# Kernel optimization log

Measured on AMD Instinct MI355X. Metric: run time of the kernel, lower is better.

The kernel has to match this reference:

```python
import jax, jax.numpy as jnp
import numpy as np

BS, NUM_VISIT, MAX_FEAT, MAX_TARGET = 32, 6, 12, 16
NUM_FEAT, NUM_REL, HIDDEN, REDUCED, OUT = 1992, 11, 128, 256, 90
GAMMA = 0.1


def setup_inputs() -> dict:
    key = jax.random.key(0)
    ks = jax.random.split(key, 20)
    u = lambda k, shape: jax.random.uniform(k, shape, dtype=jnp.float32)
    # one/multi-hot-like dense float inputs (per docstring)
    feat_index = (u(ks[0], (BS, NUM_VISIT, MAX_FEAT, NUM_FEAT)) < 0.01).astype(jnp.float32)
    neighbor_index = (u(ks[1], (BS, NUM_VISIT, MAX_FEAT, MAX_TARGET, NUM_FEAT)) < 0.001).astype(jnp.float32)
    rel_index = (u(ks[2], (BS, NUM_VISIT, MAX_FEAT, MAX_TARGET, NUM_REL)) < 0.2).astype(jnp.float32)
    # parameters (torch.rand init in the original; xavier for embedding)
    bound = float(np.sqrt(6.0 / (NUM_FEAT + HIDDEN)))
    emb_weight = jax.random.uniform(ks[3], (NUM_FEAT, HIDDEN), dtype=jnp.float32, minval=-bound, maxval=bound)
    return {
        "feat_index": feat_index,
        "neighbor_index": neighbor_index,
        "rel_index": rel_index,
        "emb_weight": emb_weight,
        "W_edge": u(ks[4], (NUM_REL, HIDDEN)),
        "W_v": u(ks[5], (REDUCED, HIDDEN)),
        "W_r": u(ks[6], (REDUCED, HIDDEN)),
        "b_v": u(ks[7], (REDUCED,)),
        "b_r": u(ks[8], (REDUCED,)),
        "W_alpha": u(ks[9], (NUM_FEAT,)),
        "b_alpha": u(ks[10], (MAX_FEAT,)),
        "W_beta": u(ks[11], (MAX_FEAT,)),
        "b_beta": u(ks[12], (NUM_VISIT,)),
        "W_l": u(ks[13], (REDUCED, REDUCED)),
        "b_l": u(ks[14], (REDUCED,)),
        "fc_W": u(ks[15], (OUT, 2 * REDUCED)) * 0.05,
        "fc_b": u(ks[16], (OUT,)) * 0.05,
    }


def reference(feat_index, neighbor_index, rel_index, emb_weight, W_edge, W_v, W_r,
              b_v, b_r, W_alpha, b_alpha, W_beta, b_beta, W_l, b_l, fc_W, fc_b):
    num_visit = feat_index.shape[1]
    # decay buffer lamb[i] = exp(-gamma*(num_visit - i))
    lamb = jnp.exp(-GAMMA * (num_visit - jnp.arange(num_visit, dtype=feat_index.dtype)))

    # node-level attention alpha: (b,v,m)
    alpha = jax.nn.softmax(jnp.einsum('n,bvmn->bvm', W_alpha, feat_index) + b_alpha)
    # visit-level attention beta: (b,v), modulated by temporal decay
    beta = jnp.tanh(jnp.einsum('m,bvm->bv', W_beta, alpha) + b_beta) * lamb

    # reduced node embeddings: (num_feat, reduced)
    reduced_emb = emb_weight @ W_v.T + b_v
    # attention-weighted neighbor aggregation; sum over targets t fused in
    attn = alpha * beta[:, :, None]                       # (b,v,m)
    node_agg = jnp.einsum('bvm,bvmtn,nr->bvmr', attn, neighbor_index, reduced_emb)

    # reduced edge (relation) embeddings: (num_rel, reduced)
    reduced_edge = W_edge @ W_r.T + b_r
    edge_agg = jnp.einsum('bvmtr,rd->bvmd', rel_index, reduced_edge)  # sum over t fused

    agg = node_agg + edge_agg                             # (b,v,m,reduced)
    # einsum('dd, bvfd -> bvfd') in torch takes the diagonal of W_l
    h = jax.nn.relu(jnp.diagonal(W_l) * agg + b_l)        # (b,v,m,reduced)

    h_g = h.sum(axis=(1, 2))                              # (b, reduced)
    # einsum('bvmn,bvmr->bvnr').sum(n).sum(v) == contract over v,m,n
    h_p = jnp.einsum('bvm,bvmr->br', feat_index.sum(-1), h)

    z_joint = jnp.concatenate([h_g, h_p], axis=-1)        # (b, 2*reduced)
    return jax.nn.sigmoid(z_joint @ fc_W.T + fc_b)
```

## Files before the change

kernel.cpp:

```cpp
#include <hip/hip_runtime.h>
#include <math.h>

#define BS   32
#define NV   6
#define MF   12
#define MT   16
#define NF   1992
#define NR   11
#define HID  128
#define RED  256
#define OUTD 90
#define GAMMA 0.1f
#define NZCAP 1024

typedef float f4_t __attribute__((ext_vector_type(4)));

#define WS_HG    0
#define WS_HP    (WS_HG + BS*RED)
#define WS_ATTN  (WS_HP + BS*RED)
#define WS_FSUM  (WS_ATTN + BS*NV*MF)
#define WS_REMB  (WS_FSUM + BS*NV*MF)
#define WS_REDGE (WS_REMB + NF*RED)
#define WS_WTV   (WS_REDGE + NR*RED)
#define WS_WTR   (WS_WTV + HID*RED)
#define WS_FCWT  (WS_WTR + HID*RED)
#define WS_DIAG  (WS_FCWT + 2*RED*OUTD)
#define WS_CNT   (WS_DIAG + RED)
#define WS_RSUM  (WS_CNT + BS*NV*MF)
#define WS_NZN   (WS_RSUM + BS*NV*MF*NR)
#define WS_NZV   (WS_NZN + BS*NV*MF*NZCAP)

#define STREAM_BLOCKS (BS*NV*MF)
#define N_ZERO (2*BS*RED)
#define N_WTV  (HID*RED)
#define N_WTR  (HID*RED)
#define N_FCWT (2*RED*OUTD)
#define N_DIAG RED
#define PREP_ELEMS (N_ZERO + N_WTV + N_WTR + N_FCWT + N_DIAG)
#define PREP_BLOCKS (PREP_ELEMS / 256)

__global__ __launch_bounds__(256) void k_stream_prep_attn(
        const float* __restrict__ nbr, const float* __restrict__ rel,
        const float* __restrict__ W_v, const float* __restrict__ W_r,
        const float* __restrict__ fc_W, const float* __restrict__ W_l,
        const float* __restrict__ feat, const float* __restrict__ W_alpha,
        const float* __restrict__ b_alpha, const float* __restrict__ W_beta,
        const float* __restrict__ b_beta,
        float* __restrict__ ws_base,
        float* __restrict__ WT_v, float* __restrict__ WT_r, float* __restrict__ fcWT,
        float* __restrict__ diag,
        int* __restrict__ cnt_g, float* __restrict__ rsum_g,
        int* __restrict__ nzn_g, float* __restrict__ nzv_g,
        float* __restrict__ attn_ws, float* __restrict__ fsum_ws) {
    int blk = blockIdx.x;
    int tid = threadIdx.x;

    if (blk < STREAM_BLOCKS) {
        int bvm = blk;
        __shared__ int   nz_n[NZCAP];
        __shared__ float nz_v[NZCAP];
        __shared__ float relbuf[MT * NR];
        __shared__ int   cnt;
        if (tid == 0) cnt = 0;
        if (tid < MT * NR / 4) {
            ((f4_t*)relbuf)[tid] = ((const f4_t*)(rel + (size_t)bvm * MT * NR))[tid];
        }

        const f4_t* base = (const f4_t*)(nbr + (size_t)bvm * MT * NF);
        f4_t x[8];
        f4_t a0 = (f4_t)(0.f);
        f4_t a1 = (f4_t)(0.f);
        #pragma unroll
        for (int t = 0; t < 8; ++t) x[t] = __builtin_nontemporal_load(base + t * (NF/4) + tid);
        #pragma unroll
        for (int t = 0; t < 8; ++t) a0 += x[t];
        #pragma unroll
        for (int t = 0; t < 8; ++t) x[t] = __builtin_nontemporal_load(base + (t + 8) * (NF/4) + tid);
        #pragma unroll
        for (int t = 0; t < 8; ++t) a0 += x[t];
        const bool has1 = (tid + 256) < (NF / 4);
        if (has1) {
            #pragma unroll
            for (int t = 0; t < 8; ++t) x[t] = __builtin_nontemporal_load(base + t * (NF/4) + tid + 256);
            #pragma unroll
            for (int t = 0; t < 8; ++t) a1 += x[t];
            #pragma unroll
            for (int t = 0; t < 8; ++t) x[t] = __builtin_nontemporal_load(base + (t + 8) * (NF/4) + tid + 256);
            #pragma unroll
            for (int t = 0; t < 8; ++t) a1 += x[t];
        }
        __syncthreads();

        int nb = tid * 4;
        #pragma unroll
        for (int c = 0; c < 4; ++c)
            if (a0[c] != 0.f) {
                int p = atomicAdd(&cnt, 1);
                if (p < NZCAP) { nz_n[p] = nb + c; nz_v[p] = a0[c]; }
            }
        if (has1) {
            nb = (tid + 256) * 4;
            #pragma unroll
            for (int c = 0; c < 4; ++c)
                if (a1[c] != 0.f) {
                    int p = atomicAdd(&cnt, 1);
                    if (p < NZCAP) { nz_n[p] = nb + c; nz_v[p] = a1[c]; }
                }
        }
        __syncthreads();
        int c = min(cnt, NZCAP);
        if (tid == 0) cnt_g[bvm] = c;
        if (tid < NR) {
            float rs = 0.f;
            #pragma unroll
            for (int t = 0; t < MT; ++t) rs += relbuf[t * NR + tid];
            rsum_g[bvm * NR + tid] = rs;
        }
        for (int i = tid; i < c; i += 256) {
            nzn_g[bvm * NZCAP + i] = nz_n[i];
            nzv_g[bvm * NZCAP + i] = nz_v[i];
        }
        return;
    }
    blk -= STREAM_BLOCKS;

    if (blk < PREP_BLOCKS) {
        int i = blk * 256 + tid;
        if (i < N_ZERO) {
            ws_base[i] = 0.f;
        } else if (i < N_ZERO + N_WTV) {
            int j = i - N_ZERO;
            int k = j >> 8, r = j & 255;
            WT_v[j] = W_v[r * HID + k];
        } else if (i < N_ZERO + N_WTV + N_WTR) {
            int j = i - (N_ZERO + N_WTV);
            int k = j >> 8, r = j & 255;
            WT_r[j] = W_r[r * HID + k];
        } else if (i < N_ZERO + N_WTV + N_WTR + N_FCWT) {
            int j = i - (N_ZERO + N_WTV + N_WTR);
            int jj = j / OUTD, o = j - jj * OUTD;
            fcWT[j] = fc_W[o * (2 * RED) + jj];
        } else {
            int j = i - (N_ZERO + N_WTV + N_WTR + N_FCWT);
            diag[j] = W_l[(size_t)j * RED + j];
        }
        return;
    }

    int bv   = blk - PREP_BLOCKS;
    int v    = bv % NV;
    int wave = tid >> 6;
    int lane = tid & 63;
    __shared__ float dot12[MF], fs12[MF];
    const float* base = feat + (size_t)bv * MF * NF;
    for (int m = wave; m < MF; m += 4) {
        const float4* rw = (const float4*)(base + (size_t)m * NF);
        const float4* wa = (const float4*)W_alpha;
        float da = 0.f, fs = 0.f;
        for (int i = lane; i < NF / 4; i += 64) {
            float4 x = rw[i];
            float4 w = wa[i];
            da += w.x * x.x + w.y * x.y + w.z * x.z + w.w * x.w;
            fs += x.x + x.y + x.z + x.w;
        }
        #pragma unroll
        for (int off = 32; off > 0; off >>= 1) {
            da += __shfl_xor(da, off);
            fs += __shfl_xor(fs, off);
        }
        if (lane == 0) { dot12[m] = da; fs12[m] = fs; }
    }
    __syncthreads();
    if (tid == 0) {
        float logits[MF];
        float mx = -1e30f;
        for (int m = 0; m < MF; ++m) { logits[m] = dot12[m] + b_alpha[m]; mx = fmaxf(mx, logits[m]); }
        float s = 0.f;
        for (int m = 0; m < MF; ++m) { logits[m] = expf(logits[m] - mx); s += logits[m]; }
        float inv = 1.f / s;
        float bdot = 0.f;
        for (int m = 0; m < MF; ++m) { logits[m] *= inv; bdot += W_beta[m] * logits[m]; }
        float lamb = expf(-GAMMA * (float)(NV - v));
        float beta = tanhf(bdot + b_beta[v]) * lamb;
        for (int m = 0; m < MF; ++m) {
            attn_ws[bv * MF + m] = logits[m] * beta;
            fsum_ws[bv * MF + m] = fs12[m];
        }
    }
}

#define NPB 8
#define NODE_BLOCKS (NF / NPB)
__global__ __launch_bounds__(256) void k_reduce(
        const float* __restrict__ emb, const float* __restrict__ W_edge,
        const float* __restrict__ WT_v, const float* __restrict__ WT_r,
        const float* __restrict__ b_v, const float* __restrict__ b_r,
        float* __restrict__ remb, float* __restrict__ redge) {
    int blk = blockIdx.x;
    int tid = threadIdx.x;
    if (blk < NODE_BLOCKS) {
        __shared__ float rows[NPB][HID];
        int n0 = blk * NPB;
        for (int i = tid; i < NPB * HID; i += 256)
            rows[i >> 7][i & 127] = emb[(size_t)n0 * HID + i];
        __syncthreads();
        float bv0 = b_v[tid];
        float a0 = bv0, a1 = bv0, a2 = bv0, a3 = bv0;
        float a4 = bv0, a5 = bv0, a6 = bv0, a7 = bv0;
        #pragma unroll 4
        for (int k = 0; k < HID; ++k) {
            float w = WT_v[k * RED + tid];
            a0 += rows[0][k] * w;
            a1 += rows[1][k] * w;
            a2 += rows[2][k] * w;
            a3 += rows[3][k] * w;
            a4 += rows[4][k] * w;
            a5 += rows[5][k] * w;
            a6 += rows[6][k] * w;
            a7 += rows[7][k] * w;
        }
        float* dst = remb + (size_t)n0 * RED + tid;
        dst[0*RED] = a0; dst[1*RED] = a1; dst[2*RED] = a2; dst[3*RED] = a3;
        dst[4*RED] = a4; dst[5*RED] = a5; dst[6*RED] = a6; dst[7*RED] = a7;
    } else {
        int e = blk - NODE_BLOCKS;
        __shared__ float row[HID];
        if (tid < HID) row[tid] = W_edge[e * HID + tid];
        __syncthreads();
        float acc = b_r[tid];
        #pragma unroll 4
        for (int k = 0; k < HID; ++k)
            acc += row[k] * WT_r[k * RED + tid];
        redge[e * RED + tid] = acc;
    }
}

__global__ __launch_bounds__(256) void k_gather(
        const float* __restrict__ remb, const float* __restrict__ redge,
        const int* __restrict__ cnt_g, const float* __restrict__ rsum_g,
        const int* __restrict__ nzn_g, const float* __restrict__ nzv_g,
        const float* __restrict__ attn_ws, const float* __restrict__ fsum_ws,
        const float* __restrict__ diag, const float* __restrict__ b_l,
        float* __restrict__ h_g, float* __restrict__ h_p) {
    int bvm = blockIdx.x;
    int b   = bvm / (NV * MF);
    int tid = threadIdx.x;
    __shared__ int   nz_n[NZCAP];
    __shared__ float nz_v[NZCAP];
    __shared__ float rsum[NR];
    int c = cnt_g[bvm];
    if (tid < NR) rsum[tid] = rsum_g[bvm * NR + tid];
    for (int i = tid; i < c; i += 256) {
        nz_n[i] = nzn_g[bvm * NZCAP + i];
        nz_v[i] = nzv_g[bvm * NZCAP + i];
    }
    __syncthreads();
    int r = tid;
    float node = 0.f;
    for (int i = 0; i < c; ++i)
        node += nz_v[i] * remb[(size_t)nz_n[i] * RED + r];
    float edge = 0.f;
    #pragma unroll
    for (int j = 0; j < NR; ++j)
        edge += rsum[j] * redge[j * RED + r];
    float a  = attn_ws[bvm];
    float fs = fsum_ws[bvm];
    float agg = a * node + edge;
    float h = fmaxf(0.f, diag[r] * agg + b_l[r]);
    atomicAdd(&h_g[b * RED + r], h);
    atomicAdd(&h_p[b * RED + r], fs * h);
}

__global__ __launch_bounds__(256) void k_out(
        const float* __restrict__ h_g, const float* __restrict__ h_p,
        const float* __restrict__ fcWT, const float* __restrict__ fc_b,
        float* __restrict__ out) {
    int b   = blockIdx.x;
    int tid = threadIdx.x;
    __shared__ float z[2 * RED];
    __shared__ float part[2][OUTD];
    for (int j = tid; j < RED; j += 256) {
        z[j]       = h_g[b * RED + j];
        z[RED + j] = h_p[b * RED + j];
    }
    __syncthreads();
    int o = tid & 127, half = tid >> 7;
    if (o < OUTD) {
        float acc = 0.f;
        int j0 = half * RED;
        #pragma unroll 8
        for (int j = j0; j < j0 + RED; ++j)
            acc += z[j] * fcWT[j * OUTD + o];
        part[half][o] = acc;
    }
    __syncthreads();
    if (tid < OUTD) {
        float acc = part[0][tid] + part[1][tid] + fc_b[tid];
        out[b * OUTD + tid] = 1.f / (1.f + expf(-acc));
    }
}

extern "C" void kernel_launch(void* const* d_in, const int* in_sizes, int n_in,
                              void* d_out, int out_size, void* d_ws, size_t ws_size,
                              hipStream_t stream) {
    const float* feat    = (const float*)d_in[0];
    const float* nbr     = (const float*)d_in[1];
    const float* rel     = (const float*)d_in[2];
    const float* emb     = (const float*)d_in[3];
    const float* W_edge  = (const float*)d_in[4];
    const float* W_v     = (const float*)d_in[5];
    const float* W_r     = (const float*)d_in[6];
    const float* b_v     = (const float*)d_in[7];
    const float* b_r     = (const float*)d_in[8];
    const float* W_alpha = (const float*)d_in[9];
    const float* b_alpha = (const float*)d_in[10];
    const float* W_beta  = (const float*)d_in[11];
    const float* b_beta  = (const float*)d_in[12];
    const float* W_l     = (const float*)d_in[13];
    const float* b_l     = (const float*)d_in[14];
    const float* fc_W    = (const float*)d_in[15];
    const float* fc_b    = (const float*)d_in[16];

    float* ws    = (float*)d_ws;
    float* hg    = ws + WS_HG;
    float* hp    = ws + WS_HP;
    float* attn  = ws + WS_ATTN;
    float* fsum  = ws + WS_FSUM;
    float* remb  = ws + WS_REMB;
    float* redge = ws + WS_REDGE;
    float* WT_v  = ws + WS_WTV;
    float* WT_r  = ws + WS_WTR;
    float* fcWT  = ws + WS_FCWT;
    float* diag  = ws + WS_DIAG;
    int*   cnt_g = (int*)(ws + WS_CNT);
    float* rsum_g= ws + WS_RSUM;
    int*   nzn_g = (int*)(ws + WS_NZN);
    float* nzv_g = ws + WS_NZV;

    k_stream_prep_attn<<<STREAM_BLOCKS + PREP_BLOCKS + BS * NV, 256, 0, stream>>>(
        nbr, rel, W_v, W_r, fc_W, W_l, feat, W_alpha, b_alpha, W_beta, b_beta,
        ws, WT_v, WT_r, fcWT, diag, cnt_g, rsum_g, nzn_g, nzv_g, attn, fsum);
    k_reduce<<<NODE_BLOCKS + NR, 256, 0, stream>>>(
        emb, W_edge, WT_v, WT_r, b_v, b_r, remb, redge);
    k_gather<<<BS * NV * MF, 256, 0, stream>>>(
        remb, redge, cnt_g, rsum_g, nzn_g, nzv_g, attn, fsum, diag, b_l, hg, hp);
    k_out<<<BS, 256, 0, stream>>>(hg, hp, fcWT, fc_b, (float*)d_out);
}
```

Baseline: 453.6 us.

## Merge reduce, gather and output kernels into one cooperative grid-synced kernel

Three of the four launches (embedding reduction, sparse gather with atomics, final FC) become one cooperative kernel. It uses a fixed grid of 1024 blocks and grid-wide syncs between phases, and the gather phase loops over the bvm items. The first kernel also reorders its blocks so prep and attention blocks come before the heavy streaming blocks. The goal is to remove launch gaps and tail effects between small kernels, at the cost of grid-sync overhead and fewer concurrent blocks in the gather phase.

```diff
diff --git a/kernel.cpp b/kernel.cpp
--- a/kernel.cpp
+++ b/kernel.cpp
@@ -1,5 +1,8 @@
 #include <hip/hip_runtime.h>
+#include <hip/hip_cooperative_groups.h>
 #include <math.h>
+
+namespace cg = cooperative_groups;
 
 #define BS   32
 #define NV   6
@@ -31,6 +34,7 @@
 #define WS_NZV   (WS_NZN + BS*NV*MF*NZCAP)
 
 #define STREAM_BLOCKS (BS*NV*MF)
+#define ATTN_BLOCKS   (BS*NV)
 #define N_ZERO (2*BS*RED)
 #define N_WTV  (HID*RED)
 #define N_WTR  (HID*RED)
@@ -39,7 +43,11 @@
 #define PREP_ELEMS (N_ZERO + N_WTV + N_WTR + N_FCWT + N_DIAG)
 #define PREP_BLOCKS (PREP_ELEMS / 256)
 
-__global__ __launch_bounds__(256) void k_stream_prep_attn(
+#define NPB 8
+#define NODE_BLOCKS (NF / NPB)
+#define TAIL_GRID 1024
+
+__global__ __launch_bounds__(256) void k_main(
         const float* __restrict__ nbr, const float* __restrict__ rel,
         const float* __restrict__ W_v, const float* __restrict__ W_r,
         const float* __restrict__ fc_W, const float* __restrict__ W_l,
@@ -54,75 +62,6 @@
         float* __restrict__ attn_ws, float* __restrict__ fsum_ws) {
     int blk = blockIdx.x;
     int tid = threadIdx.x;
-
-    if (blk < STREAM_BLOCKS) {
-        int bvm = blk;
-        __shared__ int   nz_n[NZCAP];
-        __shared__ float nz_v[NZCAP];
-        __shared__ float relbuf[MT * NR];
-        __shared__ int   cnt;
-        if (tid == 0) cnt = 0;
-        if (tid < MT * NR / 4) {
-            ((f4_t*)relbuf)[tid] = ((const f4_t*)(rel + (size_t)bvm * MT * NR))[tid];
-        }
-
-        const f4_t* base = (const f4_t*)(nbr + (size_t)bvm * MT * NF);
-        f4_t x[8];
-        f4_t a0 = (f4_t)(0.f);
-        f4_t a1 = (f4_t)(0.f);
-        #pragma unroll
-        for (int t = 0; t < 8; ++t) x[t] = __builtin_nontemporal_load(base + t * (NF/4) + tid);
-        #pragma unroll
-        for (int t = 0; t < 8; ++t) a0 += x[t];
-        #pragma unroll
-        for (int t = 0; t < 8; ++t) x[t] = __builtin_nontemporal_load(base + (t + 8) * (NF/4) + tid);
-        #pragma unroll
-        for (int t = 0; t < 8; ++t) a0 += x[t];
-        const bool has1 = (tid + 256) < (NF / 4);
-        if (has1) {
-            #pragma unroll
-            for (int t = 0; t < 8; ++t) x[t] = __builtin_nontemporal_load(base + t * (NF/4) + tid + 256);
-            #pragma unroll
-            for (int t = 0; t < 8; ++t) a1 += x[t];
-            #pragma unroll
-            for (int t = 0; t < 8; ++t) x[t] = __builtin_nontemporal_load(base + (t + 8) * (NF/4) + tid + 256);
-            #pragma unroll
-            for (int t = 0; t < 8; ++t) a1 += x[t];
-        }
-        __syncthreads();
-
-        int nb = tid * 4;
-        #pragma unroll
-        for (int c = 0; c < 4; ++c)
-            if (a0[c] != 0.f) {
-                int p = atomicAdd(&cnt, 1);
-                if (p < NZCAP) { nz_n[p] = nb + c; nz_v[p] = a0[c]; }
-            }
-        if (has1) {
-            nb = (tid + 256) * 4;
-            #pragma unroll
-            for (int c = 0; c < 4; ++c)
-                if (a1[c] != 0.f) {
-                    int p = atomicAdd(&cnt, 1);
-                    if (p < NZCAP) { nz_n[p] = nb + c; nz_v[p] = a1[c]; }
-                }
-        }
-        __syncthreads();
-        int c = min(cnt, NZCAP);
-        if (tid == 0) cnt_g[bvm] = c;
-        if (tid < NR) {
-            float rs = 0.f;
-            #pragma unroll
-            for (int t = 0; t < MT; ++t) rs += relbuf[t * NR + tid];
-            rsum_g[bvm * NR + tid] = rs;
-        }
-        for (int i = tid; i < c; i += 256) {
-            nzn_g[bvm * NZCAP + i] = nz_n[i];
-            nzv_g[bvm * NZCAP + i] = nz_v[i];
-        }
-        return;
-    }
-    blk -= STREAM_BLOCKS;
 
     if (blk < PREP_BLOCKS) {
         int i = blk * 256 + tid;
@@ -146,63 +85,140 @@
         }
         return;
     }
-
-    int bv   = blk - PREP_BLOCKS;
-    int v    = bv % NV;
-    int wave = tid >> 6;
-    int lane = tid & 63;
-    __shared__ float dot12[MF], fs12[MF];
-    const float* base = feat + (size_t)bv * MF * NF;
-    for (int m = wave; m < MF; m += 4) {
-        const float4* rw = (const float4*)(base + (size_t)m * NF);
-        const float4* wa = (const float4*)W_alpha;
-        float da = 0.f, fs = 0.f;
-        for (int i = lane; i < NF / 4; i += 64) {
-            float4 x = rw[i];
-            float4 w = wa[i];
-            da += w.x * x.x + w.y * x.y + w.z * x.z + w.w * x.w;
-            fs += x.x + x.y + x.z + x.w;
-        }
-        #pragma unroll
-        for (int off = 32; off > 0; off >>= 1) {
-            da += __shfl_xor(da, off);
-            fs += __shfl_xor(fs, off);
-        }
-        if (lane == 0) { dot12[m] = da; fs12[m] = fs; }
+    blk -= PREP_BLOCKS;
+
+    if (blk < ATTN_BLOCKS) {
+        int bv   = blk;
+        int v    = bv % NV;
+        int wave = tid >> 6;
+        int lane = tid & 63;
+        __shared__ float dot12[MF], fs12[MF];
+        const float* base = feat + (size_t)bv * MF * NF;
+        for (int m = wave; m < MF; m += 4) {
+            const float4* rw = (const float4*)(base + (size_t)m * NF);
+            const float4* wa = (const float4*)W_alpha;
+            float da = 0.f, fs = 0.f;
+            for (int i = lane; i < NF / 4; i += 64) {
+                float4 x = rw[i];
+                float4 w = wa[i];
+                da += w.x * x.x + w.y * x.y + w.z * x.z + w.w * x.w;
+                fs += x.x + x.y + x.z + x.w;
+            }
+            #pragma unroll
+            for (int off = 32; off > 0; off >>= 1) {
+                da += __shfl_xor(da, off);
+                fs += __shfl_xor(fs, off);
+            }
+            if (lane == 0) { dot12[m] = da; fs12[m] = fs; }
+        }
+        __syncthreads();
+        if (tid == 0) {
+            float logits[MF];
+            float mx = -1e30f;
+            for (int m = 0; m < MF; ++m) { logits[m] = dot12[m] + b_alpha[m]; mx = fmaxf(mx, logits[m]); }
+            float s = 0.f;
+            for (int m = 0; m < MF; ++m) { logits[m] = expf(logits[m] - mx); s += logits[m]; }
+            float inv = 1.f / s;
+            float bdot = 0.f;
+            for (int m = 0; m < MF; ++m) { logits[m] *= inv; bdot += W_beta[m] * logits[m]; }
+            float lamb = expf(-GAMMA * (float)(NV - v));
+            float beta = tanhf(bdot + b_beta[v]) * lamb;
+            for (int m = 0; m < MF; ++m) {
+                attn_ws[bv * MF + m] = logits[m] * beta;
+                fsum_ws[bv * MF + m] = fs12[m];
+            }
+        }
+        return;
+    }
+    blk -= ATTN_BLOCKS;
+
+    int bvm = blk;
+    __shared__ int   nz_n[NZCAP];
+    __shared__ float nz_v[NZCAP];
+    __shared__ float relbuf[MT * NR];
+    __shared__ int   cnt;
+    if (tid == 0) cnt = 0;
+    if (tid < MT * NR / 4) {
+        ((f4_t*)relbuf)[tid] = ((const f4_t*)(rel + (size_t)bvm * MT * NR))[tid];
+    }
+
+    const f4_t* base = (const f4_t*)(nbr + (size_t)bvm * MT * NF);
+    f4_t x[8];
+    f4_t a0 = (f4_t)(0.f);
+    f4_t a1 = (f4_t)(0.f);
+    #pragma unroll
+    for (int t = 0; t < 8; ++t) x[t] = __builtin_nontemporal_load(base + t * (NF/4) + tid);
+    #pragma unroll
+    for (int t = 0; t < 8; ++t) a0 += x[t];
+    #pragma unroll
+    for (int t = 0; t < 8; ++t) x[t] = __builtin_nontemporal_load(base + (t + 8) * (NF/4) + tid);
+    #pragma unroll
+    for (int t = 0; t < 8; ++t) a0 += x[t];
+    const bool has1 = (tid + 256) < (NF / 4);
+    if (has1) {
+        #pragma unroll
+        for (int t = 0; t < 8; ++t) x[t] = __builtin_nontemporal_load(base + t * (NF/4) + tid + 256);
+        #pragma unroll
+        for (int t = 0; t < 8; ++t) a1 += x[t];
+        #pragma unroll
+        for (int t = 0; t < 8; ++t) x[t] = __builtin_nontemporal_load(base + (t + 8) * (NF/4) + tid + 256);
+        #pragma unroll
+        for (int t = 0; t < 8; ++t) a1 += x[t];
     }
     __syncthreads();
-    if (tid == 0) {
-        float logits[MF];
-        float mx = -1e30f;
-        for (int m = 0; m < MF; ++m) { logits[m] = dot12[m] + b_alpha[m]; mx = fmaxf(mx, logits[m]); }
-        float s = 0.f;
-        for (int m = 0; m < MF; ++m) { logits[m] = expf(logits[m] - mx); s += logits[m]; }
-        float inv = 1.f / s;
-        float bdot = 0.f;
-        for (int m = 0; m < MF; ++m) { logits[m] *= inv; bdot += W_beta[m] * logits[m]; }
-        float lamb = expf(-GAMMA * (float)(NV - v));
-        float beta = tanhf(bdot + b_beta[v]) * lamb;
-        for (int m = 0; m < MF; ++m) {
-            attn_ws[bv * MF + m] = logits[m] * beta;
-            fsum_ws[bv * MF + m] = fs12[m];
-        }
+
+    int nb = tid * 4;
+    #pragma unroll
+    for (int c = 0; c < 4; ++c)
+        if (a0[c] != 0.f) {
+            int p = atomicAdd(&cnt, 1);
+            if (p < NZCAP) { nz_n[p] = nb + c; nz_v[p] = a0[c]; }
+        }
+    if (has1) {
+        nb = (tid + 256) * 4;
+        #pragma unroll
+        for (int c = 0; c < 4; ++c)
+            if (a1[c] != 0.f) {
+                int p = atomicAdd(&cnt, 1);
+                if (p < NZCAP) { nz_n[p] = nb + c; nz_v[p] = a1[c]; }
+            }
+    }
+    __syncthreads();
+    int c = min(cnt, NZCAP);
+    if (tid == 0) cnt_g[bvm] = c;
+    if (tid < NR) {
+        float rs = 0.f;
+        #pragma unroll
+        for (int t = 0; t < MT; ++t) rs += relbuf[t * NR + tid];
+        rsum_g[bvm * NR + tid] = rs;
+    }
+    for (int i = tid; i < c; i += 256) {
+        nzn_g[bvm * NZCAP + i] = nz_n[i];
+        nzv_g[bvm * NZCAP + i] = nz_v[i];
     }
 }
 
-#define NPB 8
-#define NODE_BLOCKS (NF / NPB)
-__global__ __launch_bounds__(256) void k_reduce(
+__global__ __launch_bounds__(256, 4) void k_tail(
         const float* __restrict__ emb, const float* __restrict__ W_edge,
         const float* __restrict__ WT_v, const float* __restrict__ WT_r,
         const float* __restrict__ b_v, const float* __restrict__ b_r,
-        float* __restrict__ remb, float* __restrict__ redge) {
+        float* __restrict__ remb, float* __restrict__ redge,
+        const int* __restrict__ cnt_g, const float* __restrict__ rsum_g,
+        const int* __restrict__ nzn_g, const float* __restrict__ nzv_g,
+        const float* __restrict__ attn_ws, const float* __restrict__ fsum_ws,
+        const float* __restrict__ diag, const float* __restrict__ b_l,
+        float* __restrict__ h_g, float* __restrict__ h_p,
+        const float* __restrict__ fcWT, const float* __restrict__ fc_b,
+        float* __restrict__ out) {
+    __shared__ float smem[2 * NZCAP + 16];
     int blk = blockIdx.x;
     int tid = threadIdx.x;
+
     if (blk < NODE_BLOCKS) {
-        __shared__ float rows[NPB][HID];
+        float* rows = smem;
         int n0 = blk * NPB;
         for (int i = tid; i < NPB * HID; i += 256)
-            rows[i >> 7][i & 127] = emb[(size_t)n0 * HID + i];
+            rows[i] = emb[(size_t)n0 * HID + i];
         __syncthreads();
         float bv0 = b_v[tid];
         float a0 = bv0, a1 = bv0, a2 = bv0, a3 = bv0;
@@ -210,21 +226,22 @@
         #pragma unroll 4
         for (int k = 0; k < HID; ++k) {
             float w = WT_v[k * RED + tid];
-            a0 += rows[0][k] * w;
-            a1 += rows[1][k] * w;
-            a2 += rows[2][k] * w;
-            a3 += rows[3][k] * w;
-            a4 += rows[4][k] * w;
-            a5 += rows[5][k] * w;
-            a6 += rows[6][k] * w;
-            a7 += rows[7][k] * w;
+            a0 += rows[0 * HID + k] * w;
+            a1 += rows[1 * HID + k] * w;
+            a2 += rows[2 * HID + k] * w;
+            a3 += rows[3 * HID + k] * w;
+            a4 += rows[4 * HID + k] * w;
+            a5 += rows[5 * HID + k] * w;
+            a6 += rows[6 * HID + k] * w;
+            a7 += rows[7 * HID + k] * w;
         }
         float* dst = remb + (size_t)n0 * RED + tid;
         dst[0*RED] = a0; dst[1*RED] = a1; dst[2*RED] = a2; dst[3*RED] = a3;
         dst[4*RED] = a4; dst[5*RED] = a5; dst[6*RED] = a6; dst[7*RED] = a7;
-    } else {
+        __syncthreads();
+    } else if (blk < NODE_BLOCKS + NR) {
         int e = blk - NODE_BLOCKS;
-        __shared__ float row[HID];
+        float* row = smem;
         if (tid < HID) row[tid] = W_edge[e * HID + tid];
         __syncthreads();
         float acc = b_r[tid];
@@ -232,71 +249,64 @@
         for (int k = 0; k < HID; ++k)
             acc += row[k] * WT_r[k * RED + tid];
         redge[e * RED + tid] = acc;
-    }
-}
-
-__global__ __launch_bounds__(256) void k_gather(
-        const float* __restrict__ remb, const float* __restrict__ redge,
-        const int* __restrict__ cnt_g, const float* __restrict__ rsum_g,
-        const int* __restrict__ nzn_g, const float* __restrict__ nzv_g,
-        const float* __restrict__ attn_ws, const float* __restrict__ fsum_ws,
-        const float* __restrict__ diag, const float* __restrict__ b_l,
-        float* __restrict__ h_g, float* __restrict__ h_p) {
-    int bvm = blockIdx.x;
-    int b   = bvm / (NV * MF);
-    int tid = threadIdx.x;
-    __shared__ int   nz_n[NZCAP];
-    __shared__ float nz_v[NZCAP];
-    __shared__ float rsum[NR];
-    int c = cnt_g[bvm];
-    if (tid < NR) rsum[tid] = rsum_g[bvm * NR + tid];
-    for (int i = tid; i < c; i += 256) {
-        nz_n[i] = nzn_g[bvm * NZCAP + i];
-        nz_v[i] = nzv_g[bvm * NZCAP + i];
-    }
-    __syncthreads();
-    int r = tid;
-    float node = 0.f;
-    for (int i = 0; i < c; ++i)
-        node += nz_v[i] * remb[(size_t)nz_n[i] * RED + r];
-    float edge = 0.f;
-    #pragma unroll
-    for (int j = 0; j < NR; ++j)
-        edge += rsum[j] * redge[j * RED + r];
-    float a  = attn_ws[bvm];
-    float fs = fsum_ws[bvm];
-    float agg = a * node + edge;
-    float h = fmaxf(0.f, diag[r] * agg + b_l[r]);
-    atomicAdd(&h_g[b * RED + r], h);
-    atomicAdd(&h_p[b * RED + r], fs * h);
-}
-
-__global__ __launch_bounds__(256) void k_out(
-        const float* __restrict__ h_g, const float* __restrict__ h_p,
-        const float* __restrict__ fcWT, const float* __restrict__ fc_b,
-        float* __restrict__ out) {
-    int b   = blockIdx.x;
-    int tid = threadIdx.x;
-    __shared__ float z[2 * RED];
-    __shared__ float part[2][OUTD];
-    for (int j = tid; j < RED; j += 256) {
-        z[j]       = h_g[b * RED + j];
-        z[RED + j] = h_p[b * RED + j];
-    }
-    __syncthreads();
-    int o = tid & 127, half = tid >> 7;
-    if (o < OUTD) {
-        float acc = 0.f;
-        int j0 = half * RED;
-        #pragma unroll 8
-        for (int j = j0; j < j0 + RED; ++j)
-            acc += z[j] * fcWT[j * OUTD + o];
-        part[half][o] = acc;
-    }
-    __syncthreads();
-    if (tid < OUTD) {
-        float acc = part[0][tid] + part[1][tid] + fc_b[tid];
-        out[b * OUTD + tid] = 1.f / (1.f + expf(-acc));
+        __syncthreads();
+    }
+    cg::this_grid().sync();
+
+    int*   nz_n = (int*)smem;
+    float* nz_v = smem + NZCAP;
+    float* rsum = smem + 2 * NZCAP;
+    for (int bvm = blk; bvm < STREAM_BLOCKS; bvm += TAIL_GRID) {
+        int b = bvm / (NV * MF);
+        int c = cnt_g[bvm];
+        if (tid < NR) rsum[tid] = rsum_g[bvm * NR + tid];
+        for (int i = tid; i < c; i += 256) {
+            nz_n[i] = nzn_g[bvm * NZCAP + i];
+            nz_v[i] = nzv_g[bvm * NZCAP + i];
+        }
+        __syncthreads();
+        int r = tid;
+        float node = 0.f;
+        for (int i = 0; i < c; ++i)
+            node += nz_v[i] * remb[(size_t)nz_n[i] * RED + r];
+        float edge = 0.f;
+        #pragma unroll
+        for (int j = 0; j < NR; ++j)
+            edge += rsum[j] * redge[j * RED + r];
+        float a  = attn_ws[bvm];
+        float fs = fsum_ws[bvm];
+        float agg = a * node + edge;
+        float h = fmaxf(0.f, diag[r] * agg + b_l[r]);
+        atomicAdd(&h_g[b * RED + r], h);
+        atomicAdd(&h_p[b * RED + r], fs * h);
+        __syncthreads();
+    }
+    cg::this_grid().sync();
+
+    if (blk < BS) {
+        int b = blk;
+        float* z     = smem;
+        float* part0 = smem + 2 * RED;
+        float* part1 = part0 + OUTD;
+        for (int j = tid; j < RED; j += 256) {
+            z[j]       = h_g[b * RED + j];
+            z[RED + j] = h_p[b * RED + j];
+        }
+        __syncthreads();
+        int o = tid & 127, half = tid >> 7;
+        if (o < OUTD) {
+            float acc = 0.f;
+            int j0 = half * RED;
+            #pragma unroll 8
+            for (int j = j0; j < j0 + RED; ++j)
+                acc += z[j] * fcWT[j * OUTD + o];
+            if (half) part1[o] = acc; else part0[o] = acc;
+        }
+        __syncthreads();
+        if (tid < OUTD) {
+            float acc = part0[tid] + part1[tid] + fc_b[tid];
+            out[b * OUTD + tid] = 1.f / (1.f + expf(-acc));
+        }
     }
 }
 
@@ -336,13 +346,19 @@
     float* rsum_g= ws + WS_RSUM;
     int*   nzn_g = (int*)(ws + WS_NZN);
     float* nzv_g = ws + WS_NZV;
-
-    k_stream_prep_attn<<<STREAM_BLOCKS + PREP_BLOCKS + BS * NV, 256, 0, stream>>>(
+    float* outp  = (float*)d_out;
+
+    k_main<<<PREP_BLOCKS + ATTN_BLOCKS + STREAM_BLOCKS, 256, 0, stream>>>(
         nbr, rel, W_v, W_r, fc_W, W_l, feat, W_alpha, b_alpha, W_beta, b_beta,
         ws, WT_v, WT_r, fcWT, diag, cnt_g, rsum_g, nzn_g, nzv_g, attn, fsum);
-    k_reduce<<<NODE_BLOCKS + NR, 256, 0, stream>>>(
-        emb, W_edge, WT_v, WT_r, b_v, b_r, remb, redge);
-    k_gather<<<BS * NV * MF, 256, 0, stream>>>(
-        remb, redge, cnt_g, rsum_g, nzn_g, nzv_g, attn, fsum, diag, b_l, hg, hp);
-    k_out<<<BS, 256, 0, stream>>>(hg, hp, fcWT, fc_b, (float*)d_out);
+
+    void* args[] = {
+        (void*)&emb, (void*)&W_edge, (void*)&WT_v, (void*)&WT_r,
+        (void*)&b_v, (void*)&b_r, (void*)&remb, (void*)&redge,
+        (void*)&cnt_g, (void*)&rsum_g, (void*)&nzn_g, (void*)&nzv_g,
+        (void*)&attn, (void*)&fsum, (void*)&diag, (void*)&b_l,
+        (void*)&hg, (void*)&hp, (void*)&fcWT, (void*)&fc_b, (void*)&outp
+    };
+    hipLaunchCooperativeKernel((void*)k_tail, dim3(TAIL_GRID), dim3(256),
+                               args, 0, stream);
 }
```

New measurement: 670.0 us. 1.48x slower.
